# Kernel tuning notes

Hardware: AMD Instinct MI355X
Metric: run time of the kernel (lower is better)

## Reference

```python
import jax, jax.numpy as jnp
import numpy as np

B, S = 64, 512
NUM_C = 1000
SKILL_DIM = ANSWER_DIM = HIDDEN = 256
ATTN_DIM = 80
LSTM_IN = SKILL_DIM + ANSWER_DIM  # 512


def setup_inputs() -> dict:
    key = jax.random.key(0)
    ks = jax.random.split(key, 12)
    sc = 0.05
    return {
        "skill": jax.random.randint(ks[0], (B, S), 0, NUM_C),
        "answer": jax.random.randint(ks[1], (B, S), 0, 2),
        "skill_emb": jax.random.normal(ks[2], (NUM_C + 1, SKILL_DIM), jnp.float32) * sc,
        "answer_emb": jax.random.normal(ks[3], (3, ANSWER_DIM), jnp.float32) * sc,
        "Wih": jax.random.normal(ks[4], (4 * HIDDEN, LSTM_IN), jnp.float32) * sc,
        "Whh": jax.random.normal(ks[5], (4 * HIDDEN, HIDDEN), jnp.float32) * sc,
        "bih": jnp.zeros((4 * HIDDEN,), jnp.float32),
        "bhh": jnp.zeros((4 * HIDDEN,), jnp.float32),
        "mlp_W": jax.random.normal(ks[6], (ATTN_DIM, HIDDEN), jnp.float32) * sc,
        "mlp_b": jnp.zeros((ATTN_DIM,), jnp.float32),
        "sim_W": jax.random.normal(ks[7], (1, ATTN_DIM), jnp.float32) * sc,
        "fc_W": jax.random.normal(ks[8], (NUM_C, 2 * HIDDEN), jnp.float32) * sc,
        "fc_b": jnp.zeros((NUM_C,), jnp.float32),
    }


def _lstm(x, Wih, Whh, bih, bhh):
    # x: [B, S, In] -> h_seq: [B, S, H]. PyTorch gate order: i, f, g, o.
    Bsz = x.shape[0]
    H = Whh.shape[1]
    x_t = jnp.swapaxes(x, 0, 1)  # [S, B, In]
    xproj = x_t @ Wih.T + (bih + bhh)  # precompute input projection [S, B, 4H]

    def step(carry, xp):
        h, c = carry
        gates = xp + h @ Whh.T
        i, f, g, o = jnp.split(gates, 4, axis=-1)
        i, f, o = jax.nn.sigmoid(i), jax.nn.sigmoid(f), jax.nn.sigmoid(o)
        g = jnp.tanh(g)
        c = f * c + i * g
        h = o * jnp.tanh(c)
        return (h, c), h

    init = (jnp.zeros((Bsz, H), x.dtype), jnp.zeros((Bsz, H), x.dtype))
    _, hs = jax.lax.scan(step, init, xproj)
    return jnp.swapaxes(hs, 0, 1)  # [B, S, H]


def reference(skill, answer, skill_emb, answer_emb, Wih, Whh, bih, bhh,
              mlp_W, mlp_b, sim_W, fc_W, fc_b):
    se = skill_emb[skill]    # [B, S, Ds]
    ae = answer_emb[answer]  # [B, S, Da]
    skill_answer = jnp.concatenate([se, ae], axis=2)
    answer_skill = jnp.concatenate([ae, se], axis=2)
    cond = (answer == 1)[:, :, None]
    sa_emb = jnp.where(cond, skill_answer, answer_skill)  # [B, S, In]

    out = _lstm(sa_emb, Wih, Whh, bih, bhh)  # [B, S, H]

    # attention_module (fix=True path)
    att = jnp.tanh(out @ mlp_W.T + mlp_b) @ sim_W.T  # [B, S, 1]
    att = att[:, :, 0]  # [B, S] (score of each key position)
    seq = att.shape[1]
    # causal mask: position i attends to j <= i; strictly-upper entries -> -inf
    mask = jnp.triu(jnp.ones((seq, seq), bool), k=1)
    scores = jnp.where(mask[None, :, :], -jnp.inf, att[:, None, :])  # [B, S, S]
    alphas = jax.nn.softmax(scores, axis=-1)
    attn_out = jnp.einsum('bij,bjh->bih', alphas, out)  # [B, S, H]
    attn_cum_1 = jnp.cumsum(attn_out, axis=1) - attn_out
    final = jnp.concatenate([attn_cum_1, out], axis=2)  # [B, S, 2H]

    res = jax.nn.sigmoid(final @ fc_W.T + fc_b)  # [B, S, num_c]
    return res, sa_emb
```

## Files before the change

kernel.cpp:

```cpp
#include <hip/hip_runtime.h>


typedef _Float16 half8 __attribute__((ext_vector_type(8)));
typedef float f32x4 __attribute__((ext_vector_type(4)));

#define BS 32768
#define NC 1000

__device__ __forceinline__ float sigm(float x) {
    return __builtin_amdgcn_rcpf(1.f + __expf(-x));
}
__device__ __forceinline__ float tanh_(float x) {
    float e = __expf(2.f * x);
    return 1.f - 2.f * __builtin_amdgcn_rcpf(e + 1.f);
}

__global__ void prep_kernel(const float* __restrict__ Wih, const float* __restrict__ fcW,
                            const float* __restrict__ mlpW, const float* __restrict__ se,
                            const float* __restrict__ ae, const float* __restrict__ bih,
                            const float* __restrict__ bhh,
                            _Float16* __restrict__ wih16, _Float16* __restrict__ fcw16,
                            _Float16* __restrict__ mlpw16, _Float16* __restrict__ se16,
                            float* __restrict__ bsum, float* __restrict__ qvec) {
    int i = blockIdx.x * 256 + threadIdx.x;
    if (i < 524288) {
        wih16[i] = (_Float16)Wih[i];
    } else if (i < 1048576) {
        int j = i - 524288;
        int r = j >> 9;
        fcw16[j] = (r < NC) ? (_Float16)fcW[j] : (_Float16)0.f;
    } else if (i < 1081344) {
        int j = i - 1048576;
        int r = j >> 8;
        mlpw16[j] = (r < 80) ? (_Float16)mlpW[j] : (_Float16)0.f;
    } else if (i < 1337600) {
        int j = i - 1081344;
        se16[j] = (_Float16)se[j];
    } else if (i < 1338624) {
        int j = i - 1337600;
        bsum[j] = bih[j] + bhh[j];
    } else if (i < 1340672) {
        int j = i - 1338624;
        int which = j >> 10, col = j & 1023;
        int aerow = (which == 0) ? 1 : 0;
        int koff  = (which == 0) ? 256 : 0;
        float s = 0.f;
        for (int k = 0; k < 256; k++)
            s += ae[aerow * 256 + k] * Wih[(size_t)col * 512 + koff + k];
        qvec[j] = s + bih[col] + bhh[col];
    }
}

__global__ void embed_kernel(const int* __restrict__ skill, const int* __restrict__ answer,
                             const float* __restrict__ se, const float* __restrict__ ae,
                             float* __restrict__ sa_out, int* __restrict__ ridx) {
    int token = blockIdx.x;
    int sk = skill[token], an = answer[token];
    const float* first  = (an == 1) ? (se + (size_t)sk * 256) : (ae + (size_t)an * 256);
    const float* second = (an == 1) ? (ae + (size_t)an * 256) : (se + (size_t)sk * 256);
    int j = threadIdx.x * 4;
    const float* src = (j < 256) ? (first + j) : (second + (j - 256));
    float4 v = *(const float4*)src;
    *(float4*)(sa_out + (size_t)token * 512 + j) = v;
    if (threadIdx.x == 0) ridx[token] = (an == 1) ? sk : (1024 + sk);
}

__global__ __launch_bounds__(256) void tgemm_kernel(
        const _Float16* __restrict__ A, const _Float16* __restrict__ Bw,
        const float* __restrict__ qvec, _Float16* __restrict__ Tsw) {
    int bm = blockIdx.x * 128, bn = blockIdx.y * 128;
    int which = bm >> 10;
    int mbase = bm & 1023;
    int koff = which ? 256 : 0;
    int tid = threadIdx.x, wv = tid >> 6, lane = tid & 63;
    int quad = lane >> 4, l16 = lane & 15;
    int wm = (wv & 1) * 64, wn = (wv >> 1) * 64;

    int arow[4];
#pragma unroll
    for (int i = 0; i < 4; i++) {
        int r = mbase + wm + i * 16 + l16;
        arow[i] = (r > 1000) ? 1000 : r;
    }
    const _Float16* Bbase = Bw + (size_t)(bn + wn + l16) * 512 + koff + quad * 8;

    f32x4 acc[4][4] = {};
    for (int kk = 0; kk < 256; kk += 32) {
        half8 a[4], b[4];
#pragma unroll
        for (int i = 0; i < 4; i++)
            a[i] = *(const half8*)(A + (size_t)arow[i] * 256 + quad * 8 + kk);
#pragma unroll
        for (int j = 0; j < 4; j++)
            b[j] = *(const half8*)(Bbase + (size_t)j * 16 * 512 + kk);
#pragma unroll
        for (int i = 0; i < 4; i++)
#pragma unroll
            for (int j = 0; j < 4; j++)
                acc[i][j] = __builtin_amdgcn_mfma_f32_16x16x32_f16(a[i], b[j], acc[i][j], 0, 0, 0);
    }
#pragma unroll
    for (int j = 0; j < 4; j++) {
        int col = bn + wn + j * 16 + l16;
        float qv = qvec[which * 1024 + col];
        int perm = ((col & 255) >> 5) * 128 + (col & 15) * 8 + ((col >> 8) * 2 + ((col >> 4) & 1));
#pragma unroll
        for (int i = 0; i < 4; i++) {
            int row = mbase + wm + i * 16 + quad * 4;
#pragma unroll
            for (int r = 0; r < 4; r++) {
                if (row + r > 1000) continue;
                Tsw[(size_t)((which << 10) + row + r) * 1024 + perm] = (_Float16)(acc[i][j][r] + qv);
            }
        }
    }
}

__global__ __launch_bounds__(512, 2) void lstm_kernel(
        const float* __restrict__ Whh,
        const _Float16* __restrict__ Tsw,
        const int* __restrict__ ridxArr,
        _Float16* __restrict__ outH) {
    int bid = blockIdx.x;
    int tid = threadIdx.x, wv = tid >> 6, lane = tid & 63;
    int quad = lane >> 4, l16 = lane & 15;
    int row = lane >> 5;
    int hc  = lane & 31;

    extern __shared__ char smem[];
    _Float16* ldsB = (_Float16*)smem;
    _Float16* hA   = (_Float16*)(smem + 131072);
    float*    rd   = (float*)(smem + 147456);

    half8 rB[48];
#pragma unroll
    for (int v = 0; v < 8; v++) {
#pragma unroll
        for (int k = 0; k < 8; k++) {
            int col = (v >> 1) * 256 + wv * 32 + (v & 1) * 16 + l16;
            const float* p = Whh + (size_t)col * 256 + k * 32 + quad * 8;
            float4 x0 = *(const float4*)p;
            float4 x1 = *(const float4*)(p + 4);
            half8 hb;
            hb[0] = (_Float16)x0.x; hb[1] = (_Float16)x0.y; hb[2] = (_Float16)x0.z; hb[3] = (_Float16)x0.w;
            hb[4] = (_Float16)x1.x; hb[5] = (_Float16)x1.y; hb[6] = (_Float16)x1.z; hb[7] = (_Float16)x1.w;
            if (k < 6) rB[k * 8 + v] = hb;
            else *(half8*)(ldsB + ((size_t)wv * 16 + (k - 6) * 8 + v) * 512 + lane * 8) = hb;
        }
    }
#pragma unroll
    for (int z = tid; z < 1024; z += 512)
        ((float4*)hA)[z] = float4{0.f, 0.f, 0.f, 0.f};

    int b0 = bid * 2 + row;
    int tb = b0 * 512;
    _Float16* po = outH + (size_t)b0 * 512 * 256 + wv * 32 + hc;

    float c = 0.f;
    half8 Tcur;
    unsigned ridxA;
    {
        int r0 = ridxArr[tb];
        Tcur = *(const half8*)(Tsw + (size_t)r0 * 1024 + wv * 128 + (hc & 15) * 8);
        ridxA = ridxArr[tb + 1];
    }
    __syncthreads();

    int cur = 0;
    for (int t = 0; t < 512; t++) {
        int tn2 = (t + 2 < 512) ? t + 2 : 511;
        half8 Tnx = *(const half8*)(Tsw + (size_t)ridxA * 1024 + wv * 128 + (hc & 15) * 8);
        unsigned ridxB = ridxArr[tb + tn2];

        f32x4 acc[8];
#pragma unroll
        for (int v = 0; v < 8; v++) acc[v] = f32x4{0.f, 0.f, 0.f, 0.f};

        const _Float16* hAc = hA + cur * 4096;
#pragma unroll
        for (int k = 0; k < 8; k++) {
            half8 av = *(const half8*)(hAc + k * 512 + lane * 8);
#pragma unroll
            for (int v = 0; v < 8; v++) {
                half8 bv;
                if (k < 6) bv = rB[k * 8 + v];
                else bv = *(const half8*)(ldsB + ((size_t)wv * 16 + (k - 6) * 8 + v) * 512 + lane * 8);
                acc[v] = __builtin_amdgcn_mfma_f32_16x16x32_f16(av, bv, acc[v], 0, 0, 0);
            }
        }

        if (quad == 0) {
#pragma unroll
            for (int r2 = 0; r2 < 2; r2++)
#pragma unroll
                for (int par = 0; par < 2; par++) {
                    f32x4 pv;
                    pv[0] = acc[0 + par][r2];
                    pv[1] = acc[2 + par][r2];
                    pv[2] = acc[4 + par][r2];
                    pv[3] = acc[6 + par][r2];
                    *(f32x4*)(rd + wv * 256 + r2 * 128 + l16 * 8 + par * 4) = pv;
                }
        }
        int pr = hc >> 4;
        f32x4 pa = *(const f32x4*)(rd + wv * 256 + row * 128 + (hc & 15) * 8 + pr * 4);

        float tg0 = pr ? (float)Tcur[1] : (float)Tcur[0];
        float tg1 = pr ? (float)Tcur[3] : (float)Tcur[2];
        float tg2 = pr ? (float)Tcur[5] : (float)Tcur[4];
        float tg3 = pr ? (float)Tcur[7] : (float)Tcur[6];

        float ii = sigm(pa[0] + tg0);
        float ff = sigm(pa[1] + tg1);
        float gg = tanh_(pa[2] + tg2);
        float oo = sigm(pa[3] + tg3);
        c = ff * c + ii * gg;
        float h = oo * tanh_(c);
        _Float16 hf = (_Float16)h;

        hA[(cur ^ 1) * 4096 + wv * 512 + (hc >> 3) * 128 + row * 8 + (hc & 7)] = hf;

        __syncthreads();
        cur ^= 1;

        po[0] = hf;
        po += 256;
        Tcur = Tnx;
        ridxA = ridxB;
    }
}

__global__ __launch_bounds__(256) void gemm_f16(
        const _Float16* __restrict__ A, const _Float16* __restrict__ Bw,
        const float* __restrict__ bias, float* __restrict__ C,
        int K, int ldC, int Nstore, int epi) {
    int bm = blockIdx.x * 128, bn = blockIdx.y * 128;
    int tid = threadIdx.x, wv = tid >> 6, lane = tid & 63;
    int quad = lane >> 4, l16 = lane & 15;
    int wm = (wv & 1) * 64, wn = (wv >> 1) * 64;

    const _Float16* Abase = A + (size_t)(bm + wm + l16) * K + quad * 8;
    const _Float16* Bbase = Bw + (size_t)(bn + wn + l16) * K + quad * 8;

    f32x4 acc[4][4] = {};
    for (int kk = 0; kk < K; kk += 32) {
        half8 a[4], b[4];
#pragma unroll
        for (int i = 0; i < 4; i++) a[i] = *(const half8*)(Abase + (size_t)i * 16 * K + kk);
#pragma unroll
        for (int j = 0; j < 4; j++) b[j] = *(const half8*)(Bbase + (size_t)j * 16 * K + kk);
#pragma unroll
        for (int i = 0; i < 4; i++)
#pragma unroll
            for (int j = 0; j < 4; j++)
                acc[i][j] = __builtin_amdgcn_mfma_f32_16x16x32_f16(a[i], b[j], acc[i][j], 0, 0, 0);
    }
#pragma unroll
    for (int j = 0; j < 4; j++) {
        int col = bn + wn + j * 16 + l16;
        if (col >= Nstore) continue;
        float bv = bias ? bias[col] : 0.f;
#pragma unroll
        for (int i = 0; i < 4; i++) {
            int row0 = bm + wm + i * 16 + quad * 4;
#pragma unroll
            for (int r = 0; r < 4; r++) {
                float v = acc[i][j][r] + bv;
                if (epi == 1) v = sigm(v);
                C[(size_t)(row0 + r) * ldC + col] = v;
            }
        }
    }
}

__global__ void att_kernel(const float* __restrict__ mlpout, const float* __restrict__ simW,
                           float* __restrict__ att) {
    int m = blockIdx.x * 256 + threadIdx.x;
    float s = 0.f;
#pragma unroll
    for (int d = 0; d < 80; d += 4) {
        float4 v = *(const float4*)(mlpout + (size_t)m * 80 + d);
        float4 w = *(const float4*)(simW + d);
        s += tanh_(v.x) * w.x + tanh_(v.y) * w.y + tanh_(v.z) * w.z + tanh_(v.w) * w.w;
    }
    att[m] = s;
}

__global__ __launch_bounds__(256) void scan_kernel(const float* __restrict__ att,
                                                   const _Float16* __restrict__ outH,
                                                   _Float16* __restrict__ finalB) {
    int b = blockIdx.x, d = threadIdx.x;
    __shared__ float w_s[512];
    for (int i = d; i < 512; i += 256) w_s[i] = __expf(att[(size_t)b * 512 + i]);
    __syncthreads();

    float S = 0.f, W = 0.f, C = 0.f;
    const _Float16* op = outH + (size_t)b * 512 * 256 + d;
    _Float16* fp = finalB + (size_t)b * 512 * 512 + d;
    for (int i = 0; i < 512; i++) {
        float w = w_s[i];
        float ov = (float)op[(size_t)i * 256];
        S += w * ov;
        W += w;
        float ao = S * __builtin_amdgcn_rcpf(W);
        fp[(size_t)i * 512]       = (_Float16)C;
        fp[(size_t)i * 512 + 256] = (_Float16)ov;
        C += ao;
    }
}

extern "C" void kernel_launch(void* const* d_in, const int* in_sizes, int n_in,
                              void* d_out, int out_size, void* d_ws, size_t ws_size,
                              hipStream_t stream) {
    const int*   skill      = (const int*)d_in[0];
    const int*   answer     = (const int*)d_in[1];
    const float* skill_emb  = (const float*)d_in[2];
    const float* answer_emb = (const float*)d_in[3];
    const float* Wih        = (const float*)d_in[4];
    const float* Whh        = (const float*)d_in[5];
    const float* bih        = (const float*)d_in[6];
    const float* bhh        = (const float*)d_in[7];
    const float* mlp_W      = (const float*)d_in[8];
    const float* mlp_b      = (const float*)d_in[9];
    const float* sim_W      = (const float*)d_in[10];
    const float* fc_W       = (const float*)d_in[11];
    const float* fc_b       = (const float*)d_in[12];

    float* res    = (float*)d_out;
    float* sa_out = res + (size_t)BS * NC;

    char* ws = (char*)d_ws;
    _Float16* outH   = (_Float16*)(ws);
    _Float16* finalB = (_Float16*)(ws + 16777216);
    _Float16* wih16  = (_Float16*)(ws + 50331648);
    _Float16* fcw16  = (_Float16*)(ws + 51380224);
    _Float16* mlpw16 = (_Float16*)(ws + 52428800);
    _Float16* se16   = (_Float16*)(ws + 52494336);
    float*    bsum   = (float*)(ws + 53018624);
    float*    qvec   = (float*)(ws + 53022720);
    float*    att    = (float*)(ws + 53030912);
    float*    mlpout = (float*)(ws + 53161984);
    _Float16* Tsw    = (_Float16*)(ws + 63647744);
    int*      ridx   = (int*)(ws + 67842048);

    (void)bsum; (void)in_sizes; (void)n_in; (void)out_size; (void)ws_size;

    hipLaunchKernelGGL(prep_kernel, dim3(5238), dim3(256), 0, stream,
                       Wih, fc_W, mlp_W, skill_emb, answer_emb, bih, bhh,
                       wih16, fcw16, mlpw16, se16, bsum, qvec);
    hipLaunchKernelGGL(embed_kernel, dim3(BS), dim3(128), 0, stream,
                       skill, answer, skill_emb, answer_emb, sa_out, ridx);
    hipLaunchKernelGGL(tgemm_kernel, dim3(16, 8), dim3(256), 0, stream,
                       se16, wih16, qvec, Tsw);

    hipFuncSetAttribute((const void*)lstm_kernel,
                        hipFuncAttributeMaxDynamicSharedMemorySize, 155648);
    hipLaunchKernelGGL(lstm_kernel, dim3(32), dim3(512), 155648, stream,
                       Whh, Tsw, ridx, outH);

    hipLaunchKernelGGL(gemm_f16, dim3(256, 1), dim3(256), 0, stream,
                       outH, mlpw16, mlp_b, mlpout, 256, 80, 80, 0);
    hipLaunchKernelGGL(att_kernel, dim3(128), dim3(256), 0, stream, mlpout, sim_W, att);
    hipLaunchKernelGGL(scan_kernel, dim3(64), dim3(256), 0, stream, att, outH, finalB);
    hipLaunchKernelGGL(gemm_f16, dim3(256, 8), dim3(256), 0, stream,
                       finalB, fcw16, fc_b, res, 512, 1000, 1000, 1);
}
```

Measured before the change: 1.312 ms.

## Compact LSTM hidden-state LDS layout and permute gate table for half4 loads

Replaces the padded 16-row hidden-state A buffer with a compact two-row layout. Lanes beyond the two real batch rows read a shared zero region, so each step writes and reads far less LDS. The input-projection table is re-permuted so each lane loads one half4 holding its own four gates instead of a half8 plus selects, and the reduction scratch layout is reorganized. LDS allocation shrinks, at the cost of more complex addressing and bank-conflict behavior that is hard to predict for the broadcast zero reads.

```diff
diff --git a/kernel.cpp b/kernel.cpp
--- a/kernel.cpp
+++ b/kernel.cpp
@@ -2,6 +2,7 @@
 
 
 typedef _Float16 half8 __attribute__((ext_vector_type(8)));
+typedef _Float16 half4 __attribute__((ext_vector_type(4)));
 typedef float f32x4 __attribute__((ext_vector_type(4)));
 
 #define BS 32768
@@ -103,7 +104,7 @@
     for (int j = 0; j < 4; j++) {
         int col = bn + wn + j * 16 + l16;
         float qv = qvec[which * 1024 + col];
-        int perm = ((col & 255) >> 5) * 128 + (col & 15) * 8 + ((col >> 8) * 2 + ((col >> 4) & 1));
+        int perm = ((col & 255) >> 5) * 128 + (((col >> 4) & 1)) * 64 + (col & 15) * 4 + (col >> 8);
 #pragma unroll
         for (int i = 0; i < 4; i++) {
             int row = mbase + wm + i * 16 + quad * 4;
@@ -126,11 +127,11 @@
     int quad = lane >> 4, l16 = lane & 15;
     int row = lane >> 5;
     int hc  = lane & 31;
+    int pr = hc >> 4, hcLow = hc & 15;
 
     extern __shared__ char smem[];
     _Float16* ldsB = (_Float16*)smem;
-    _Float16* hA   = (_Float16*)(smem + 131072);
-    float*    rd   = (float*)(smem + 147456);
+    float*    rd   = (float*)(smem + 133152);
 
     half8 rB[48];
 #pragma unroll
@@ -148,20 +149,23 @@
             else *(half8*)(ldsB + ((size_t)wv * 16 + (k - 6) * 8 + v) * 512 + lane * 8) = hb;
         }
     }
-#pragma unroll
-    for (int z = tid; z < 1024; z += 512)
-        ((float4*)hA)[z] = float4{0.f, 0.f, 0.f, 0.f};
+    if (tid < 130) ((float4*)(smem + 131072))[tid] = float4{0.f, 0.f, 0.f, 0.f};
 
     int b0 = bid * 2 + row;
     int tb = b0 * 512;
     _Float16* po = outH + (size_t)b0 * 512 * 256 + wv * 32 + hc;
 
+    bool realA = (l16 < 2);
+    int hb0 = realA ? (131072 + l16 * 512 + quad * 16) : 133120;
+    int hb1 = realA ? (131072 + 1024 + l16 * 512 + quad * 16) : 133120;
+    int kstep = realA ? 64 : 0;
+
     float c = 0.f;
-    half8 Tcur;
+    half4 Tcur;
     unsigned ridxA;
     {
         int r0 = ridxArr[tb];
-        Tcur = *(const half8*)(Tsw + (size_t)r0 * 1024 + wv * 128 + (hc & 15) * 8);
+        Tcur = *(const half4*)(Tsw + (size_t)r0 * 1024 + wv * 128 + pr * 64 + hcLow * 4);
         ridxA = ridxArr[tb + 1];
     }
     __syncthreads();
@@ -169,17 +173,18 @@
     int cur = 0;
     for (int t = 0; t < 512; t++) {
         int tn2 = (t + 2 < 512) ? t + 2 : 511;
-        half8 Tnx = *(const half8*)(Tsw + (size_t)ridxA * 1024 + wv * 128 + (hc & 15) * 8);
+        half4 Tnx = *(const half4*)(Tsw + (size_t)ridxA * 1024 + wv * 128 + pr * 64 + hcLow * 4);
         unsigned ridxB = ridxArr[tb + tn2];
 
         f32x4 acc[8];
 #pragma unroll
         for (int v = 0; v < 8; v++) acc[v] = f32x4{0.f, 0.f, 0.f, 0.f};
 
-        const _Float16* hAc = hA + cur * 4096;
+        const char* hp = smem + (cur ? hb1 : hb0);
 #pragma unroll
         for (int k = 0; k < 8; k++) {
-            half8 av = *(const half8*)(hAc + k * 512 + lane * 8);
+            half8 av = *(const half8*)hp;
+            hp += kstep;
 #pragma unroll
             for (int v = 0; v < 8; v++) {
                 half8 bv;
@@ -199,26 +204,20 @@
                     pv[1] = acc[2 + par][r2];
                     pv[2] = acc[4 + par][r2];
                     pv[3] = acc[6 + par][r2];
-                    *(f32x4*)(rd + wv * 256 + r2 * 128 + l16 * 8 + par * 4) = pv;
+                    *(f32x4*)(rd + wv * 256 + (par * 32 + r2 * 16 + l16) * 4) = pv;
                 }
         }
-        int pr = hc >> 4;
-        f32x4 pa = *(const f32x4*)(rd + wv * 256 + row * 128 + (hc & 15) * 8 + pr * 4);
-
-        float tg0 = pr ? (float)Tcur[1] : (float)Tcur[0];
-        float tg1 = pr ? (float)Tcur[3] : (float)Tcur[2];
-        float tg2 = pr ? (float)Tcur[5] : (float)Tcur[4];
-        float tg3 = pr ? (float)Tcur[7] : (float)Tcur[6];
-
-        float ii = sigm(pa[0] + tg0);
-        float ff = sigm(pa[1] + tg1);
-        float gg = tanh_(pa[2] + tg2);
-        float oo = sigm(pa[3] + tg3);
+        f32x4 pa = *(const f32x4*)(rd + wv * 256 + (pr * 32 + row * 16 + hcLow) * 4);
+
+        float ii = sigm(pa[0] + (float)Tcur[0]);
+        float ff = sigm(pa[1] + (float)Tcur[1]);
+        float gg = tanh_(pa[2] + (float)Tcur[2]);
+        float oo = sigm(pa[3] + (float)Tcur[3]);
         c = ff * c + ii * gg;
         float h = oo * tanh_(c);
         _Float16 hf = (_Float16)h;
 
-        hA[(cur ^ 1) * 4096 + wv * 512 + (hc >> 3) * 128 + row * 8 + (hc & 7)] = hf;
+        *(_Float16*)(smem + 131072 + ((cur ^ 1) << 10) + (row << 9) + (wv * 32 + hc) * 2) = hf;
 
         __syncthreads();
         cur ^= 1;
@@ -354,8 +353,8 @@
                        se16, wih16, qvec, Tsw);
 
     hipFuncSetAttribute((const void*)lstm_kernel,
-                        hipFuncAttributeMaxDynamicSharedMemorySize, 155648);
-    hipLaunchKernelGGL(lstm_kernel, dim3(32), dim3(512), 155648, stream,
+                        hipFuncAttributeMaxDynamicSharedMemorySize, 141344);
+    hipLaunchKernelGGL(lstm_kernel, dim3(32), dim3(512), 141344, stream,
                        Whh, Tsw, ridx, outH);
 
     hipLaunchKernelGGL(gemm_f16, dim3(256, 1), dim3(256), 0, stream,
```

After: 1.369 ms. 4.3% more time.
